# Performance work log

Measured on AMD Instinct MI355X. Metric: run time of the kernel, lower is better.

The kernel has to match this reference:

```python
import jax, jax.numpy as jnp
import numpy as np

N_CUST, N_PROD, D, H, OUT, E = 100000, 10000, 128, 128, 64, 500000
RELS = ["purchase", "redeem", "transfer_to", "transfer_from", "dividend_from"]


def setup_inputs() -> dict:
    key = jax.random.key(0)
    ks = jax.random.split(key, 40)
    inp = {}
    inp["x_cust"] = jax.random.normal(ks[0], (N_CUST, D), jnp.float32)
    inp["x_prod"] = jax.random.normal(ks[1], (N_PROD, D), jnp.float32)
    for i, r in enumerate(RELS):
        inp["src_" + r] = jax.random.randint(ks[2 + 2 * i], (E,), 0, N_CUST)
        inp["dst_" + r] = jax.random.randint(ks[3 + 2 * i], (E,), 0, N_PROD)
    s = 0.05
    names = [("W_gcn", (D, H)), ("b_gcn", (H,)), ("Ws_gat", (D, H)), ("Wd_gat", (D, H)),
             ("a_s_gat", (H,)), ("a_d_gat", (H,)), ("b_gat", (H,)),
             ("Wl_to", (D, H)), ("b_to", (H,)), ("Wr_to", (D, H)),
             ("Wl_from", (D, H)), ("b_from", (H,)), ("Wr_from", (D, H)),
             ("Wl_div", (D, H)), ("b_div", (H,)), ("Wr_div", (D, H)),
             ("W_out", (H, OUT)), ("b_out", (OUT,))]
    for i, (n, shp) in enumerate(names):
        inp[n] = jax.random.normal(ks[12 + i], shp, jnp.float32) * s
    return inp


def _gcn(x_src, src, dst, W, b):
    # symmetric-norm bipartite GCN: transform then gather->scale->scatter
    deg_s = jax.ops.segment_sum(jnp.ones_like(src, jnp.float32), src, N_CUST)
    deg_d = jax.ops.segment_sum(jnp.ones_like(dst, jnp.float32), dst, N_PROD)
    norm = jax.lax.rsqrt(deg_s[src] * deg_d[dst])  # [E]
    h = x_src @ W  # [N_CUST, H]
    return jax.ops.segment_sum(norm[:, None] * h[src], dst, N_PROD) + b


def _gat(x_src, x_dst, src, dst, Ws, Wd, a_s, a_d, b):
    # single-head bipartite GAT with edge-softmax over incoming edges at dst
    hs = x_src @ Ws                     # [N_CUST, H]
    ls = hs @ a_s                       # [N_CUST]
    ld = (x_dst @ Wd) @ a_d             # [N_PROD]
    logit = jax.nn.leaky_relu(ls[src] + ld[dst], 0.2)  # [E]
    m = jax.ops.segment_max(logit, dst, N_PROD)
    e = jnp.exp(logit - m[dst])
    den = jax.ops.segment_sum(e, dst, N_PROD)
    alpha = e / den[dst]
    return jax.ops.segment_sum(alpha[:, None] * hs[src], dst, N_PROD) + b


def _sage(x_src, x_dst, src, dst, Wl, bl, Wr):
    # mean-aggregate raw src features, then linear; plus root transform of dst
    s = jax.ops.segment_sum(x_src[src], dst, N_PROD)
    c = jax.ops.segment_sum(jnp.ones_like(dst, jnp.float32), dst, N_PROD)
    mean = s / jnp.maximum(c, 1.0)[:, None]
    return mean @ Wl + bl + x_dst @ Wr


def reference(x_cust, x_prod, src_purchase, dst_purchase, src_redeem, dst_redeem,
              src_transfer_to, dst_transfer_to, src_transfer_from, dst_transfer_from,
              src_dividend_from, dst_dividend_from,
              W_gcn, b_gcn, Ws_gat, Wd_gat, a_s_gat, a_d_gat, b_gat,
              Wl_to, b_to, Wr_to, Wl_from, b_from, Wr_from, Wl_div, b_div, Wr_div,
              W_out, b_out):
    prod = _gcn(x_cust, src_purchase, dst_purchase, W_gcn, b_gcn)
    prod = prod + _gat(x_cust, x_prod, src_redeem, dst_redeem, Ws_gat, Wd_gat, a_s_gat, a_d_gat, b_gat)
    prod = prod + _sage(x_cust, x_prod, src_transfer_to, dst_transfer_to, Wl_to, b_to, Wr_to)
    prod = prod + _sage(x_cust, x_prod, src_transfer_from, dst_transfer_from, Wl_from, b_from, Wr_from)
    prod = prod + _sage(x_cust, x_prod, src_dividend_from, dst_dividend_from, Wl_div, b_div, Wr_div)
    prod = jax.nn.relu(prod)  # HeteroConv(aggr='sum') then relu
    return prod @ W_out + b_out  # [N_PROD, OUT]
```

## Files before the change

### kernel.cpp

```cpp
#include <hip/hip_runtime.h>

#define WF 64
#define CAP 128
#define CH 2048
#define LC 32
#define NGMAX 160
#define BINCAP 3584

typedef int v4i __attribute__((ext_vector_type(4)));
typedef short short8 __attribute__((ext_vector_type(8)));
typedef float f32x4 __attribute__((ext_vector_type(4)));
typedef float f32x2 __attribute__((ext_vector_type(2)));

#if __has_builtin(__builtin_amdgcn_cvt_f32_fp8) && __has_builtin(__builtin_amdgcn_cvt_pk_fp8_f32)
#define HW_FP8 1
#endif

__device__ __forceinline__ void gload_lds16(const void* g, void* lds) {
    __builtin_amdgcn_global_load_lds(
        (const __attribute__((address_space(1))) unsigned int*)g,
        (__attribute__((address_space(3))) unsigned int*)lds, 16, 0, 0);
}

__device__ __forceinline__ unsigned fp8enc1(float x) {
    unsigned b = __builtin_bit_cast(unsigned, x);
    unsigned s = (b >> 24) & 0x80u;
    int E = (b >> 23) & 0xff;
    unsigned m = b & 0x7fffffu;
    unsigned mr = (m + 0x7ffffu + ((m >> 20) & 1u)) >> 20;
    int e8 = E - 120 + (int)(mr >> 3);
    mr &= 7u;
    if (e8 <= 0) return s;
    if (e8 > 15) { e8 = 15; mr = 7u; }
    return s | ((unsigned)e8 << 3) | mr;
}
__device__ __forceinline__ float fp8dec1(unsigned u8) {
    unsigned f = ((u8 & 0x80u) << 24) | (((u8 & 0x7fu) << 20) + 0x3C000000u);
    return (u8 & 0x7fu) ? __builtin_bit_cast(float, f) : 0.f;
}
__device__ __forceinline__ unsigned fp8pack4(float4 u) {
#ifdef HW_FP8
    int r = __builtin_amdgcn_cvt_pk_fp8_f32(u.x, u.y, 0, false);
    r = __builtin_amdgcn_cvt_pk_fp8_f32(u.z, u.w, r, true);
    return (unsigned)r;
#else
    return fp8enc1(u.x) | (fp8enc1(u.y) << 8) | (fp8enc1(u.z) << 16) | (fp8enc1(u.w) << 24);
#endif
}
__device__ __forceinline__ void accP2(float w, unsigned u, f32x2& A, f32x2& B) {
    f32x2 w2 = {w, w};
#if defined(HW_FP8) && __has_builtin(__builtin_amdgcn_cvt_pk_f32_fp8)
    f32x2 d0 = __builtin_amdgcn_cvt_pk_f32_fp8((int)u, false);
    f32x2 d1 = __builtin_amdgcn_cvt_pk_f32_fp8((int)u, true);
    A = __builtin_elementwise_fma(w2, d0, A);
    B = __builtin_elementwise_fma(w2, d1, B);
#elif defined(HW_FP8)
    f32x2 d0 = {__builtin_amdgcn_cvt_f32_fp8((int)u, 0), __builtin_amdgcn_cvt_f32_fp8((int)u, 1)};
    f32x2 d1 = {__builtin_amdgcn_cvt_f32_fp8((int)u, 2), __builtin_amdgcn_cvt_f32_fp8((int)u, 3)};
    A = __builtin_elementwise_fma(w2, d0, A);
    B = __builtin_elementwise_fma(w2, d1, B);
#else
    A[0] = fmaf(w, fp8dec1(u & 0xffu), A[0]);
    A[1] = fmaf(w, fp8dec1((u >> 8) & 0xffu), A[1]);
    B[0] = fmaf(w, fp8dec1((u >> 16) & 0xffu), B[0]);
    B[1] = fmaf(w, fp8dec1(u >> 24), B[1]);
#endif
}

__device__ __forceinline__ short bf16r(float x) {
    unsigned u = __builtin_bit_cast(unsigned, x);
    u += 0x7fffu + ((u >> 16) & 1u);
    return (short)(u >> 16);
}
__device__ __forceinline__ void bfsplit(float x, short& hi, short& lo) {
    unsigned u = __builtin_bit_cast(unsigned, x);
    hi = (short)(u >> 16);
    float fh = __builtin_bit_cast(float, u & 0xffff0000u);
    lo = bf16r(x - fh);
}

__global__ void k_init(int* deg_s, int nc2, int* bincur, int nb, int ZB,
                       const float* __restrict__ Ws, const float* __restrict__ Wd,
                       const float* __restrict__ as_, const float* __restrict__ ad_,
                       const float* __restrict__ bg, const float* __restrict__ bga,
                       const float* __restrict__ bto, const float* __restrict__ bfr,
                       const float* __restrict__ bdv,
                       const float* __restrict__ Wg, const float* __restrict__ Wlt,
                       const float* __restrict__ Wlf, const float* __restrict__ Wld,
                       const float* __restrict__ Wrt, const float* __restrict__ Wrf,
                       const float* __restrict__ Wrd, const float* __restrict__ Wo,
                       float* vs, float* vd, float* bsum,
                       short* wth, short* wtl, short* woth, short* wotl) {
    int b = blockIdx.x, t = threadIdx.x;
    if (b < ZB) {
        int i = b * 256 + t;
        if (i < nc2) deg_s[i] = 0;
        if (i < nb) bincur[i] = 0;
    } else if (b == ZB) {
        if (t < 128) {
            float a = 0.f, bb = 0.f;
            for (int h = 0; h < 128; ++h) {
                a += Ws[t * 128 + h] * as_[h];
                bb += Wd[t * 128 + h] * ad_[h];
            }
            vs[t] = a; vd[t] = bb;
            bsum[t] = bg[t] + bga[t] + bto[t] + bfr[t] + bdv[t];
        }
    } else if (b < ZB + 385) {
        int e = (b - ZB - 1) * 256 + t;
        int h = e / 768;
        int q = e - h * 768;
        int m = q >> 7, k = q & 127;
        int src = k * 128 + h;
        float val;
        switch (m) {
            case 0: val = Wg[src]; break;
            case 1: val = Ws[src]; break;
            case 2: val = Wlt[src]; break;
            case 3: val = Wlf[src]; break;
            case 4: val = Wld[src]; break;
            default: val = Wrt[src] + Wrf[src] + Wrd[src]; break;
        }
        short hi, lo;
        bfsplit(val, hi, lo);
        int kswz = k ^ ((h & 7) << 3);
        int idx = h * 768 + m * 128 + kswz;
        wth[idx] = hi; wtl[idx] = lo;
    } else {
        int e = (b - ZB - 385) * 256 + t;
        int o = e >> 7, k = e & 127;
        short hi, lo;
        bfsplit(Wo[k * 64 + o], hi, lo);
        woth[e] = hi; wotl[e] = lo;
    }
}

__global__ __launch_bounds__(256) void k_bin(
    const int* s0, const int* s1, const int* s2, const int* s3, const int* s4,
    const int* d0, const int* d1, const int* d2, const int* d3, const int* d4,
    int* bincur, int* gbin, int* deg_s, int E, int NP, int ng,
    int bpjE, int B0, int HB4, int CB,
    const float* __restrict__ xc, const float* __restrict__ xp,
    const float* __restrict__ vs, const float* __restrict__ vd,
    unsigned* __restrict__ xh, float* __restrict__ lsb, float* __restrict__ ldb,
    short* __restrict__ xph, short* __restrict__ xpl, int NC) {
    __shared__ int lcnt[NGMAX];
    __shared__ int lbase[NGMAX];
    __shared__ int lbin[NGMAX * LC];
    int b = blockIdx.x, t = threadIdx.x;
    if (b < B0) {
        int rel = b / bpjE;
        int blk = b - rel * bpjE;
        const int *sp, *dp;
        switch (rel) {
            case 0: sp = s0; dp = d0; break;
            case 1: sp = s1; dp = d1; break;
            case 2: sp = s2; dp = d2; break;
            case 3: sp = s3; dp = d3; break;
            default: sp = s4; dp = d4; break;
        }
        for (int i = t; i < ng; i += 256) lcnt[i] = 0;
        __syncthreads();
        int* bc = bincur + rel * ng;
        int* gb0 = gbin + (size_t)rel * ng * BINCAP;
        int start = blk * CH;
        int q0 = start + t * 8;
#pragma unroll
        for (int c = 0; c < 8; c += 4) {
            int q = q0 + c;
            if (q >= E) break;
            if (q + 3 < E) {
                v4i dv = __builtin_nontemporal_load((const v4i*)(dp + q));
                v4i sv = __builtin_nontemporal_load((const v4i*)(sp + q));
                int dd[4] = {dv.x, dv.y, dv.z, dv.w};
                int ss[4] = {sv.x, sv.y, sv.z, sv.w};
#pragma unroll
                for (int z = 0; z < 4; ++z) {
                    int bin = dd[z] >> 6;
                    int pk = (ss[z] << 6) | (dd[z] & 63);
                    int pos = atomicAdd(&lcnt[bin], 1);
                    if (pos < LC) lbin[bin * LC + pos] = pk;
                    else {
                        int g = atomicAdd(bc + bin, 1);
                        if (g < BINCAP) gb0[(size_t)bin * BINCAP + g] = pk;
                    }
                }
            } else {
                for (int i = q; i < E; ++i) {
                    int d = dp[i];
                    int bin = d >> 6;
                    int pk = (sp[i] << 6) | (d & 63);
                    int pos = atomicAdd(&lcnt[bin], 1);
                    if (pos < LC) lbin[bin * LC + pos] = pk;
                    else {
                        int g = atomicAdd(bc + bin, 1);
                        if (g < BINCAP) gb0[(size_t)bin * BINCAP + g] = pk;
                    }
                }
            }
        }
        __syncthreads();
        if (t < ng) {
            int c = min(lcnt[t], LC);
            lbase[t] = atomicAdd(bc + t, c);
        }
        __syncthreads();
        int wv = t >> 6, lane = t & 63;
        for (int bin = wv; bin < ng; bin += 4) {
            int c = min(lcnt[bin], LC);
            int gbase = lbase[bin];
            int* gp = gb0 + (size_t)bin * BINCAP;
            for (int i = lane; i < c; i += 64) {
                int g = gbase + i;
                if (g < BINCAP) gp[g] = lbin[bin * LC + i];
            }
        }
    } else if (b < B0 + HB4) {
        int q = ((b - B0) * 256 + t) * 4;
        if (q >= E) return;
        if (q + 3 < E) {
            v4i v = __builtin_nontemporal_load((const v4i*)(s0 + q));
            atomicAdd(deg_s + v.x, 1); atomicAdd(deg_s + v.y, 1);
            atomicAdd(deg_s + v.z, 1); atomicAdd(deg_s + v.w, 1);
        } else {
            for (int i = q; i < E; ++i) atomicAdd(deg_s + s0[i], 1);
        }
    } else if (b < B0 + HB4 + CB) {
        int row = (b - B0 - HB4) * 8 + (t >> 5);
        int q = t & 31;
        if (row >= NC) return;
        float4 u = *(const float4*)(xc + (size_t)row * 128 + 4 * q);
        float4 v = *(const float4*)(vs + 4 * q);
        float s = u.x * v.x + u.y * v.y + u.z * v.z + u.w * v.w;
        xh[(size_t)row * 32 + q] = fp8pack4(u);
#pragma unroll
        for (int o = 16; o; o >>= 1) s += __shfl_xor(s, o, WF);
        if (q == 0) lsb[row] = s;
    } else {
        int row = (b - B0 - HB4 - CB) * 4 + (t >> 6);
        int l = t & 63;
        if (row >= NP) return;
        const float* xr = xp + (size_t)row * 128;
        float x0 = xr[2 * l], x1 = xr[2 * l + 1];
        short h0, lo0, h1, lo1;
        bfsplit(x0, h0, lo0);
        bfsplit(x1, h1, lo1);
        ((unsigned*)(xph + (size_t)row * 128))[l] =
            (unsigned)(unsigned short)h0 | ((unsigned)(unsigned short)h1 << 16);
        ((unsigned*)(xpl + (size_t)row * 128))[l] =
            (unsigned)(unsigned short)lo0 | ((unsigned)(unsigned short)lo1 << 16);
        float s = x0 * vd[2 * l] + x1 * vd[2 * l + 1];
        for (int o = 32; o; o >>= 1) s += __shfl_down(s, o, WF);
        if (l == 0) ldb[row] = s;
    }
}

__global__ __launch_bounds__(256) void k_aggf(
    const int* __restrict__ gbin, const int* __restrict__ bincur,
    const int* __restrict__ deg_s,
    const float* __restrict__ ls, const float* __restrict__ ld,
    const unsigned* __restrict__ xh,
    short* __restrict__ aggH, short* __restrict__ aggL,
    int NP, int ng) {
    __shared__ int cnt[16];
    __shared__ int buck[16][CAP + 4];
    __shared__ float wbuf[4][CAP + 4];
    int t = threadIdx.x;
    int rel = blockIdx.x / (4 * ng);
    int rem = blockIdx.x - rel * 4 * ng;
    int grp = rem >> 2, sub = rem & 3;
    if (t < 16) cnt[t] = 0;
    __syncthreads();
    int binid = rel * ng + grp;
    int n = min(bincur[binid], BINCAP);
    const int* bsrc = gbin + (size_t)binid * BINCAP;
    for (int i = t; i < n; i += 256) {
        int e = bsrc[i];
        int lp = e & 63;
        if ((lp >> 4) == sub) {
            int li = lp & 15;
            int pos = atomicAdd(&cnt[li], 1);
            if (pos < CAP) buck[li][pos] = e >> 6;
        }
    }
    __syncthreads();
    if (t < 16) {
        int c = min(cnt[t], CAP);
        buck[t][c] = 0; buck[t][c + 1] = 0; buck[t][c + 2] = 0;
    }
    __syncthreads();

    int wv = t >> 6, l = t & 63;
    int g = l >> 4, q8 = l & 15;

    for (int r = 0; r < 4; ++r) {
        int li = r * 4 + wv;
        int p = grp * 64 + sub * 16 + li;
        bool valid = (p < NP);
        int m = valid ? min(cnt[li], CAP) : 0;

        if (rel == 0) {
            float rd = rsqrtf((float)m);
            for (int e = l; e < m; e += WF)
                wbuf[wv][e] = rsqrtf((float)deg_s[buck[li][e]]) * rd;
        } else if (rel == 1) {
            if (m > 0) {
                float ldp = ld[p];
                float ml = -3.4e38f, dl = 0.f;
                for (int e = l; e < m; e += WF) {
                    float tt = ls[buck[li][e]] + ldp;
                    tt = tt > 0.f ? tt : 0.2f * tt;
                    wbuf[wv][e] = tt;
                    if (tt > ml) { dl = dl * __expf(ml - tt) + 1.f; ml = tt; }
                    else dl += __expf(tt - ml);
                }
                for (int o = 32; o; o >>= 1) {
                    float m2 = __shfl_xor(ml, o, WF), d2 = __shfl_xor(dl, o, WF);
                    float mm = fmaxf(ml, m2);
                    dl = dl * __expf(ml - mm) + d2 * __expf(m2 - mm);
                    ml = mm;
                }
                float inv = 1.f / dl;
                for (int e = l; e < m; e += WF)
                    wbuf[wv][e] = __expf(wbuf[wv][e] - ml) * inv;
            }
        } else {
            float sc = 1.f / fmaxf((float)m, 1.f);
            for (int e = l; e < m; e += WF) wbuf[wv][e] = sc;
        }
        if (l == 0) { wbuf[wv][m] = 0.f; wbuf[wv][m + 1] = 0.f; wbuf[wv][m + 2] = 0.f; }
        __builtin_amdgcn_wave_barrier();

        f32x2 a0 = {0.f, 0.f}, a1 = {0.f, 0.f}, a2 = {0.f, 0.f}, a3 = {0.f, 0.f};
        int nq = (m + 3) >> 2;
        int j = 0;
        for (; j + 4 <= nq; j += 4) {
            int ss[4]; float wk[4]; uint2 uu[4];
#pragma unroll
            for (int z = 0; z < 4; ++z) {
                int e = 4 * (j + z) + g;
                ss[z] = buck[li][e];
                wk[z] = wbuf[wv][e];
            }
#pragma unroll
            for (int z = 0; z < 4; ++z)
                uu[z] = *(const uint2*)(xh + (size_t)ss[z] * 32 + 2 * q8);
#pragma unroll
            for (int z = 0; z < 4; ++z) {
                accP2(wk[z], uu[z].x, a0, a1);
                accP2(wk[z], uu[z].y, a2, a3);
            }
        }
        for (; j < nq; ++j) {
            int e = 4 * j + g;
            int s0 = buck[li][e];
            float w0 = wbuf[wv][e];
            uint2 u0 = *(const uint2*)(xh + (size_t)s0 * 32 + 2 * q8);
            accP2(w0, u0.x, a0, a1);
            accP2(w0, u0.y, a2, a3);
        }

#pragma unroll
        for (int o = 16; o <= 32; o <<= 1) {
            a0[0] += __shfl_xor(a0[0], o, WF); a0[1] += __shfl_xor(a0[1], o, WF);
            a1[0] += __shfl_xor(a1[0], o, WF); a1[1] += __shfl_xor(a1[1], o, WF);
            a2[0] += __shfl_xor(a2[0], o, WF); a2[1] += __shfl_xor(a2[1], o, WF);
            a3[0] += __shfl_xor(a3[0], o, WF); a3[1] += __shfl_xor(a3[1], o, WF);
        }

        if (valid && l < 16) {
            short8 hv, lv;
            short hh, ll;
            bfsplit(a0[0], hh, ll); hv[0] = hh; lv[0] = ll;
            bfsplit(a0[1], hh, ll); hv[1] = hh; lv[1] = ll;
            bfsplit(a1[0], hh, ll); hv[2] = hh; lv[2] = ll;
            bfsplit(a1[1], hh, ll); hv[3] = hh; lv[3] = ll;
            bfsplit(a2[0], hh, ll); hv[4] = hh; lv[4] = ll;
            bfsplit(a2[1], hh, ll); hv[5] = hh; lv[5] = ll;
            bfsplit(a3[0], hh, ll); hv[6] = hh; lv[6] = ll;
            bfsplit(a3[1], hh, ll); hv[7] = hh; lv[7] = ll;
            size_t base = ((size_t)rel * NP + p) * 128 + 8 * q8;
            *(short8*)(aggH + base) = hv;
            *(short8*)(aggL + base) = lv;
        }
    }
}

__global__ __launch_bounds__(256, 2) void k_gemm_out(
    const short* __restrict__ aggH, const short* __restrict__ aggL,
    const short* __restrict__ wth, const short* __restrict__ wtl,
    const short* __restrict__ woth, const short* __restrict__ wotl,
    const float* __restrict__ bsum, const float* __restrict__ bout,
    float* __restrict__ out, int NP) {
    __shared__ char smem[65536];
    short* bsh = (short*)smem;
    short* bsl = (short*)(smem + 32768);
    short (*c1h)[136] = (short(*)[136])smem;
    short (*c1l)[136] = (short(*)[136])(smem + 32768);
    int t = threadIdx.x;
    int w = t >> 6, l = t & 63;
    int lr = l & 15, lq = l >> 4;
    int kq = lq * 8;
    int row0 = blockIdx.x * 32;
    int ar[2];
#pragma unroll
    for (int hh = 0; hh < 2; ++hh) {
        int a = row0 + 16 * hh + lr;
        ar[hh] = a > NP - 1 ? NP - 1 : a;
    }

    int srow = w * 4;
    f32x4 acc[2][2] = {};

#pragma unroll
    for (int m = 0; m < 6; ++m) {
        __syncthreads();
        {
            const char* srch = (const char*)wth + m * 256;
            const char* srcl = (const char*)wtl + m * 256;
            int hb = srow + (l >> 4);
            int cb = (l & 15) * 16;
#pragma unroll
            for (int i = 0; i < 8; ++i) {
                int h = i * 16 + hb;
                gload_lds16(srch + h * 1536 + cb, (char*)bsh + (i * 16 + srow) * 256);
            }
#pragma unroll
            for (int i = 0; i < 8; ++i) {
                int h = i * 16 + hb;
                gload_lds16(srcl + h * 1536 + cb, (char*)bsl + (i * 16 + srow) * 256);
            }
        }
        __syncthreads();

#pragma unroll
        for (int hh = 0; hh < 2; ++hh) {
            const short* ahp = aggH + ((size_t)m * NP + ar[hh]) * 128;
            const short* alp = aggL + ((size_t)m * NP + ar[hh]) * 128;
#pragma unroll
            for (int kk = 0; kk < 4; ++kk) {
                int ko = kk * 32 + kq;
                short8 ah = *(const short8*)(ahp + ko);
                short8 al = *(const short8*)(alp + ko);
#pragma unroll
                for (int ci = 0; ci < 2; ++ci) {
                    int hcol = 32 * w + 16 * ci + lr;
                    int boff = hcol * 256 + ((ko * 2) ^ ((hcol & 7) << 4));
                    short8 bh = *(const short8*)((const char*)bsh + boff);
                    short8 bl = *(const short8*)((const char*)bsl + boff);
                    acc[hh][ci] = __builtin_amdgcn_mfma_f32_16x16x32_bf16(ah, bh, acc[hh][ci], 0, 0, 0);
                    acc[hh][ci] = __builtin_amdgcn_mfma_f32_16x16x32_bf16(al, bh, acc[hh][ci], 0, 0, 0);
                    acc[hh][ci] = __builtin_amdgcn_mfma_f32_16x16x32_bf16(ah, bl, acc[hh][ci], 0, 0, 0);
                }
            }
        }
    }

    __syncthreads();

#pragma unroll
    for (int hh = 0; hh < 2; ++hh)
#pragma unroll
    for (int ci = 0; ci < 2; ++ci) {
        int col = 32 * w + 16 * ci + lr;
        float bs = bsum[col];
#pragma unroll
        for (int r = 0; r < 4; ++r) {
            float v = acc[hh][ci][r] + bs;
            v = v > 0.f ? v : 0.f;
            short hi2, lo2;
            bfsplit(v, hi2, lo2);
            int rl = 16 * hh + 4 * lq + r;
            c1h[rl][col] = hi2;
            c1l[rl][col] = lo2;
        }
    }
    __syncthreads();

    f32x4 acc2[2] = {};
#pragma unroll
    for (int kb = 0; kb < 4; ++kb) {
        int kof = kb * 32 + kq;
        int o = 16 * w + lr;
        short8 b2h = *(const short8*)(woth + o * 128 + kof);
        short8 b2l = *(const short8*)(wotl + o * 128 + kof);
#pragma unroll
        for (int hh = 0; hh < 2; ++hh) {
            short8 a2h = *(const short8*)&c1h[16 * hh + lr][kof];
            short8 a2l = *(const short8*)&c1l[16 * hh + lr][kof];
            acc2[hh] = __builtin_amdgcn_mfma_f32_16x16x32_bf16(a2h, b2h, acc2[hh], 0, 0, 0);
            acc2[hh] = __builtin_amdgcn_mfma_f32_16x16x32_bf16(a2l, b2h, acc2[hh], 0, 0, 0);
            acc2[hh] = __builtin_amdgcn_mfma_f32_16x16x32_bf16(a2h, b2l, acc2[hh], 0, 0, 0);
        }
    }
    int col = 16 * w + lr;
    float bo = bout[col];
#pragma unroll
    for (int hh = 0; hh < 2; ++hh)
#pragma unroll
    for (int r = 0; r < 4; ++r) {
        int row = row0 + 16 * hh + 4 * lq + r;
        if (row < NP) out[(size_t)row * 64 + col] = acc2[hh][r] + bo;
    }
}

extern "C" void kernel_launch(void* const* d_in, const int* in_sizes, int n_in,
                              void* d_out, int out_size, void* d_ws, size_t ws_size,
                              hipStream_t stream) {
    const float* x_cust = (const float*)d_in[0];
    const float* x_prod = (const float*)d_in[1];
    const int* src_pur = (const int*)d_in[2];  const int* dst_pur = (const int*)d_in[3];
    const int* src_red = (const int*)d_in[4];  const int* dst_red = (const int*)d_in[5];
    const int* src_to  = (const int*)d_in[6];  const int* dst_to  = (const int*)d_in[7];
    const int* src_fr  = (const int*)d_in[8];  const int* dst_fr  = (const int*)d_in[9];
    const int* src_dv  = (const int*)d_in[10]; const int* dst_dv  = (const int*)d_in[11];
    const float* W_gcn = (const float*)d_in[12];
    const float* b_gcn = (const float*)d_in[13];
    const float* Ws_gat = (const float*)d_in[14]; const float* Wd_gat = (const float*)d_in[15];
    const float* a_s = (const float*)d_in[16]; const float* a_d = (const float*)d_in[17];
    const float* b_gat = (const float*)d_in[18];
    const float* Wl_to = (const float*)d_in[19]; const float* b_to = (const float*)d_in[20];
    const float* Wr_to = (const float*)d_in[21];
    const float* Wl_fr = (const float*)d_in[22]; const float* b_fr = (const float*)d_in[23];
    const float* Wr_fr = (const float*)d_in[24];
    const float* Wl_dv = (const float*)d_in[25]; const float* b_dv = (const float*)d_in[26];
    const float* Wr_dv = (const float*)d_in[27];
    const float* W_out = (const float*)d_in[28]; const float* b_out = (const float*)d_in[29];
    float* out = (float*)d_out;

    int NC = in_sizes[0] / 128;
    int NP = in_sizes[1] / 128;
    int E  = in_sizes[2];
    int ng = (NP + 63) >> 6;

    char* ws = (char*)d_ws;
    size_t off = 0;
    auto alloc = [&](size_t bytes) -> void* {
        void* p = ws + off;
        off = (off + bytes + 255) & ~(size_t)255;
        return p;
    };
    int*      deg_s  = (int*)alloc((size_t)NC * 4);
    int*      bincur = (int*)alloc((size_t)5 * NGMAX * 4);
    int*      gbin   = (int*)alloc((size_t)5 * NGMAX * BINCAP * 4);
    float*    lsb    = (float*)alloc((size_t)NC * 4);
    float*    ldb    = (float*)alloc((size_t)NP * 4);
    float*    vs     = (float*)alloc(512);
    float*    vd     = (float*)alloc(512);
    float*    bsum   = (float*)alloc(512);
    short*    wth    = (short*)alloc((size_t)98304 * 2);
    short*    wtl    = (short*)alloc((size_t)98304 * 2);
    short*    woth   = (short*)alloc((size_t)8192 * 2);
    short*    wotl   = (short*)alloc((size_t)8192 * 2);
    unsigned* xh     = (unsigned*)alloc((size_t)NC * 32 * 4);
    short*    aggH   = (short*)alloc((size_t)6 * NP * 128 * 2);
    short*    aggL   = (short*)alloc((size_t)6 * NP * 128 * 2);
    short*    xph    = aggH + (size_t)5 * NP * 128;
    short*    xpl    = aggL + (size_t)5 * NP * 128;

    int ZB = (NC + 255) / 256;
    k_init<<<ZB + 1 + 384 + 32, 256, 0, stream>>>(deg_s, NC, bincur, 5 * ng, ZB,
                                                  Ws_gat, Wd_gat, a_s, a_d,
                                                  b_gcn, b_gat, b_to, b_fr, b_dv,
                                                  W_gcn, Wl_to, Wl_fr, Wl_dv,
                                                  Wr_to, Wr_fr, Wr_dv, W_out,
                                                  vs, vd, bsum, wth, wtl, woth, wotl);

    int bpjE = (E + CH - 1) / CH;
    int bpj4 = ((E + 3) / 4 + 255) / 256;
    int B0 = 5 * bpjE, HB4 = bpj4, CB = (NC + 7) / 8, PB = (NP + 3) / 4;
    k_bin<<<B0 + HB4 + CB + PB, 256, 0, stream>>>(
        src_pur, src_red, src_to, src_fr, src_dv,
        dst_pur, dst_red, dst_to, dst_fr, dst_dv,
        bincur, gbin, deg_s, E, NP, ng, bpjE, B0, HB4, CB,
        x_cust, x_prod, vs, vd, xh, lsb, ldb, xph, xpl, NC);

    k_aggf<<<5 * ng * 4, 256, 0, stream>>>(gbin, bincur, deg_s, lsb, ldb, xh,
                                           aggH, aggL, NP, ng);

    k_gemm_out<<<(NP + 31) / 32, 256, 0, stream>>>(
        aggH, aggL, wth, wtl, woth, wotl, bsum, b_out, out, NP);
}
```

Baseline: 278.3 us.

## Double-buffer weight staging in output GEMM with split-K chunks

The weight tiles in k_gemm_out are now staged in 12 half-width K chunks instead of 6 full ones, using two ping-pong LDS buffers. The load for the next chunk is issued right after the barrier, before the MFMA work on the current chunk. This removes one barrier per step and lets the global-to-LDS copy overlap with compute. The cost is more loop iterations, and correctness relies on the barrier waiting for the asynchronous LDS loads to finish.

```diff
diff --git a/kernel.cpp b/kernel.cpp
--- a/kernel.cpp
+++ b/kernel.cpp
@@ -393,8 +393,6 @@
     const float* __restrict__ bsum, const float* __restrict__ bout,
     float* __restrict__ out, int NP) {
     __shared__ char smem[65536];
-    short* bsh = (short*)smem;
-    short* bsl = (short*)(smem + 32768);
     short (*c1h)[136] = (short(*)[136])smem;
     short (*c1l)[136] = (short(*)[136])(smem + 32768);
     int t = threadIdx.x;
@@ -409,45 +407,45 @@
         ar[hh] = a > NP - 1 ? NP - 1 : a;
     }
 
-    int srow = w * 4;
+    auto stage = [&](int c, char* buf) {
+        int m = c >> 1, hf = c & 1;
+        const char* srch = (const char*)wth + m * 256 + hf * 128 + (l & 7) * 16;
+        const char* srcl = (const char*)wtl + m * 256 + hf * 128 + (l & 7) * 16;
+        int rl8 = l >> 3;
+#pragma unroll
+        for (int i = 0; i < 4; ++i) {
+            int r0 = i * 32 + w * 8;
+            int h = r0 + rl8;
+            gload_lds16(srch + (size_t)h * 1536, buf + r0 * 128);
+            gload_lds16(srcl + (size_t)h * 1536, buf + 16384 + r0 * 128);
+        }
+    };
+
     f32x4 acc[2][2] = {};
 
-#pragma unroll
-    for (int m = 0; m < 6; ++m) {
+    stage(0, smem);
+#pragma unroll
+    for (int c = 0; c < 12; ++c) {
         __syncthreads();
-        {
-            const char* srch = (const char*)wth + m * 256;
-            const char* srcl = (const char*)wtl + m * 256;
-            int hb = srow + (l >> 4);
-            int cb = (l & 15) * 16;
-#pragma unroll
-            for (int i = 0; i < 8; ++i) {
-                int h = i * 16 + hb;
-                gload_lds16(srch + h * 1536 + cb, (char*)bsh + (i * 16 + srow) * 256);
-            }
-#pragma unroll
-            for (int i = 0; i < 8; ++i) {
-                int h = i * 16 + hb;
-                gload_lds16(srcl + h * 1536 + cb, (char*)bsl + (i * 16 + srow) * 256);
-            }
-        }
-        __syncthreads();
-
+        if (c < 11) stage(c + 1, smem + ((c + 1) & 1) * 32768);
+        int m = c >> 1, hf = c & 1;
+        const char* bsh = smem + (c & 1) * 32768;
+        const char* bsl = bsh + 16384;
 #pragma unroll
         for (int hh = 0; hh < 2; ++hh) {
-            const short* ahp = aggH + ((size_t)m * NP + ar[hh]) * 128;
-            const short* alp = aggL + ((size_t)m * NP + ar[hh]) * 128;
-#pragma unroll
-            for (int kk = 0; kk < 4; ++kk) {
+            const short* ahp = aggH + ((size_t)m * NP + ar[hh]) * 128 + hf * 64;
+            const short* alp = aggL + ((size_t)m * NP + ar[hh]) * 128 + hf * 64;
+#pragma unroll
+            for (int kk = 0; kk < 2; ++kk) {
                 int ko = kk * 32 + kq;
                 short8 ah = *(const short8*)(ahp + ko);
                 short8 al = *(const short8*)(alp + ko);
 #pragma unroll
                 for (int ci = 0; ci < 2; ++ci) {
                     int hcol = 32 * w + 16 * ci + lr;
-                    int boff = hcol * 256 + ((ko * 2) ^ ((hcol & 7) << 4));
-                    short8 bh = *(const short8*)((const char*)bsh + boff);
-                    short8 bl = *(const short8*)((const char*)bsl + boff);
+                    int boff = hcol * 128 + ((ko * 2) ^ ((hcol & 7) << 4));
+                    short8 bh = *(const short8*)(bsh + boff);
+                    short8 bl = *(const short8*)(bsl + boff);
                     acc[hh][ci] = __builtin_amdgcn_mfma_f32_16x16x32_bf16(ah, bh, acc[hh][ci], 0, 0, 0);
                     acc[hh][ci] = __builtin_amdgcn_mfma_f32_16x16x32_bf16(al, bh, acc[hh][ci], 0, 0, 0);
                     acc[hh][ci] = __builtin_amdgcn_mfma_f32_16x16x32_bf16(ah, bl, acc[hh][ci], 0, 0, 0);
```

New measurement: 277.0 us. No clear change (-0.5%).
